# Kernel optimization log

Hardware: AMD Instinct MI355X
Metric: run time of the kernel (lower is better)

## Reference

```python
import jax, jax.numpy as jnp
import numpy as np

T, N, C, S = 512, 32, 5000, 100
BLANK = 0
NEG = -1e30  # log-space 'zero'


def setup_inputs() -> dict:
    key = jax.random.key(0)
    k1, k2, k3 = jax.random.split(key, 3)
    logits = jax.random.normal(k1, (T, N, C), dtype=jnp.float32)
    log_probs = jax.nn.log_softmax(logits, axis=-1)  # CTC expects log-probs
    targets = jax.random.randint(k2, (N, S), 1, C)   # labels never equal blank(=0)
    input_lengths = jnp.full((N,), T, dtype=jnp.int32)
    target_lengths = jax.random.randint(k3, (N,), S // 2, S + 1).astype(jnp.int32)
    return {"log_probs": log_probs, "targets": targets,
            "input_lengths": input_lengths, "target_lengths": target_lengths}


def _logsumexp3(a, b, c):
    m = jnp.maximum(jnp.maximum(a, b), c)
    return m + jnp.log(jnp.exp(a - m) + jnp.exp(b - m) + jnp.exp(c - m))


def _ctc_loss(log_probs, targets, input_lengths, target_lengths, blank=BLANK):
    Tm, Nb, Cc = log_probs.shape
    Sm = targets.shape[1]
    L = 2 * Sm + 1  # extended (blank-interleaved) label lattice width

    # extended targets: [blank, t0, blank, t1, ..., blank]  -> shape [N, L]
    ext = jnp.full((Nb, L), blank, dtype=targets.dtype)
    ext = ext.at[:, 1::2].set(targets)
    is_label = (jnp.arange(L) % 2 == 1)
    ext_prev2 = jnp.concatenate(
        [jnp.full((Nb, 2), -1, dtype=ext.dtype), ext[:, :-2]], axis=1)
    allow_skip = is_label[None, :] & (ext != ext_prev2)          # [N, L]
    pos_mask = jnp.arange(L)[None, :] < (2 * target_lengths + 1)[:, None]

    def emit(lp_t):  # lp_t: [N, C] -> [N, L] gather of label log-probs
        return jnp.take_along_axis(lp_t, ext, axis=1)

    # init alpha at t=0
    e0 = emit(log_probs[0])
    alpha0 = jnp.full((Nb, L), NEG, dtype=log_probs.dtype)
    alpha0 = alpha0.at[:, 0].set(e0[:, 0])
    alpha0 = alpha0.at[:, 1].set(jnp.where(target_lengths > 0, e0[:, 1], NEG))
    alpha0 = jnp.where(pos_mask, alpha0, NEG)

    neg1 = jnp.full((Nb, 1), NEG, dtype=log_probs.dtype)
    neg2 = jnp.full((Nb, 2), NEG, dtype=log_probs.dtype)

    def step(alpha, xs):
        lp_t, t = xs
        a1 = jnp.concatenate([neg1, alpha[:, :-1]], axis=1)
        a2 = jnp.where(allow_skip,
                       jnp.concatenate([neg2, alpha[:, :-2]], axis=1), NEG)
        new = _logsumexp3(alpha, a1, a2) + emit(lp_t)
        new = jnp.where(pos_mask, new, NEG)
        active = (t < input_lengths)[:, None]  # freeze alpha past input length
        return jnp.where(active, new, alpha), None

    alpha, _ = jax.lax.scan(step, alpha0,
                            (log_probs[1:], jnp.arange(1, Tm)))

    # total log-likelihood: last blank + last label states
    last = (2 * target_lengths).astype(jnp.int32)
    a_blank = jnp.take_along_axis(alpha, last[:, None], axis=1)[:, 0]
    a_label = jnp.take_along_axis(alpha, jnp.maximum(last - 1, 0)[:, None], axis=1)[:, 0]
    m = jnp.maximum(a_blank, a_label)
    ll = m + jnp.log(jnp.exp(a_blank - m) + jnp.exp(a_label - m))
    loss = -ll
    # zero_infinity=True: zero out infinite losses
    loss = jnp.where(jnp.isfinite(loss) & (loss < 1e29), loss, 0.0)
    # reduction='mean': divide by target_lengths (clamped to 1), then batch mean
    loss = loss / jnp.maximum(target_lengths, 1).astype(loss.dtype)
    return jnp.mean(loss)


def reference(log_probs, targets, input_lengths, target_lengths):
    return _ctc_loss(log_probs, targets, input_lengths, target_lengths)
```

## Files before the change

kernel.cpp:

```cpp
#include <hip/hip_runtime.h>
#include <cstdint>
#include <cmath>

#define Tt   512
#define Nb   32
#define Cc   5000
#define Sm   100
#define NEGV (-1e30f)
#define LOG2E 1.4426950408889634f
#define LN2   0.6931471805599453f
#define TCH  8

#if __has_builtin(__builtin_amdgcn_exp2f)
#define EXP2F(x) __builtin_amdgcn_exp2f(x)
#else
#define EXP2F(x) exp2f(x)
#endif
#if __has_builtin(__builtin_amdgcn_logf)
#define LOG2F(x) __builtin_amdgcn_logf(x)
#else
#define LOG2F(x) log2f(x)
#endif

__device__ __forceinline__ float lse2_l2(float a, float b) {
    float m = fmaxf(a, b);
    return m + LOG2F(1.0f + EXP2F(fminf(a, b) - m));
}
__device__ __forceinline__ float lse3_l2(float a, float b, float c) {
    float m   = fmaxf(fmaxf(a, b), c);
    float mid = __builtin_amdgcn_fmed3f(a, b, c);
    float lo  = fminf(fminf(a, b), c);
    return m + LOG2F(1.0f + EXP2F(mid - m) + EXP2F(lo - m));
}

__global__ __launch_bounds__(128, 1)
void ctc_gather_kernel(const float* __restrict__ lp,
                       const int*   __restrict__ tgt,
                       float*       __restrict__ em2,
                       float*       __restrict__ out)
{
    const int bid = blockIdx.x;
    const int n   = bid >> 6;
    const int t0  = (bid & 63) * TCH;
    const int j   = threadIdx.x;

    if (bid == 0 && j == 127) out[0] = 0.0f;

    float* dst = em2 + (((size_t)n * Tt + t0) << 7) + j;

    if (j <= Sm) {
        const int e = (j < Sm) ? tgt[n * Sm + j] : 0;
        const float* src = lp + (size_t)n * Cc + e;
        float v[TCH];
#pragma unroll
        for (int k = 0; k < TCH; ++k)
            v[k] = src[(size_t)(t0 + k) * (Nb * Cc)];
#pragma unroll
        for (int k = 0; k < TCH; ++k)
            dst[k << 7] = v[k] * LOG2E;
    } else {
#pragma unroll
        for (int k = 0; k < TCH; ++k)
            dst[k << 7] = NEGV;
    }
}

__global__ __launch_bounds__(64, 1)
void ctc_alpha_wave_kernel(const float* __restrict__ em2,
                           const int*   __restrict__ tgt,
                           const int*   __restrict__ ilen,
                           const int*   __restrict__ tlen,
                           float*       __restrict__ out)
{
    const int n = blockIdx.x;
    const int i = threadIdx.x;

    const int tl = tlen[n];
    const int il = ilen[n];

    const int j1 = 2 * i, j3 = 2 * i + 1;
    bool s1 = false, s3 = false;
    if (j1 >= 1 && j1 < Sm) s1 = (tgt[n * Sm + j1] != tgt[n * Sm + j1 - 1]);
    if (j3 < Sm)            s3 = (tgt[n * Sm + j3] != tgt[n * Sm + j3 - 1]);

    const float2* e2 = (const float2*)em2 + ((size_t)n << 15);

    const int pull = (i > 0 ? i - 1 : 0) << 2;

    float2 E0 = e2[i];
    float b0 = __int_as_float(
        __builtin_amdgcn_readlane(__float_as_int(E0.x), 50));
    float a0 = (i == 0)           ? b0   : NEGV;
    float a1 = (i == 0 && tl > 0) ? E0.x : NEGV;
    float a2 = NEGV;
    float a3 = NEGV;

    constexpr int PF = 8;
    float2 ebuf[PF];
#pragma unroll
    for (int k = 0; k < PF; ++k)
        ebuf[k] = e2[((1 + k) << 6) + i];

    for (int tb = 1; tb < Tt; tb += PF) {
#pragma unroll
        for (int k = 0; k < PF; ++k) {
            const int t = tb + k;
            if (t < Tt) {
                float2 e  = ebuf[k];
                int    tp = t + PF;
                if (tp < Tt) ebuf[k] = e2[(tp << 6) + i];

                float eb = __int_as_float(
                    __builtin_amdgcn_readlane(__float_as_int(e.x), 50));

                float p3  = __int_as_float(
                    __builtin_amdgcn_ds_bpermute(pull, __float_as_int(a3)));
                float am0 = (i > 0) ? p3 : NEGV;

                float n0 = lse2_l2(a0, am0)                   + eb;
                float n1 = lse3_l2(a1, a0, s1 ? p3 : NEGV)    + e.x;
                float n2 = lse2_l2(a2, a1)                    + eb;
                float n3 = lse3_l2(a3, a2, s3 ? a1 : NEGV)    + e.y;

                if (t < il) {
                    a0 = n0; a1 = n1; a2 = n2; a3 = n3;
                }
            }
        }
    }

    const int lb = 2 * tl;
    const int lv = (lb - 1 >= 0) ? lb - 1 : 0;

    int   cb = lb & 3;
    float vb = (cb == 0) ? a0 : (cb == 1) ? a1 : (cb == 2) ? a2 : a3;
    float ab = __shfl(vb, lb >> 2);
    int   cl = lv & 3;
    float vl = (cl == 0) ? a0 : (cl == 1) ? a1 : (cl == 2) ? a2 : a3;
    float al = __shfl(vl, lv >> 2);

    if (i == 0) {
        float m    = fmaxf(ab, al);
        float ll2  = m + LOG2F(EXP2F(ab - m) + EXP2F(al - m));
        float loss = -ll2 * LN2;
        if (!(isfinite(loss) && loss < 1e29f)) loss = 0.0f;
        int   d    = (tl >= 1) ? tl : 1;
        atomicAdd(out, loss / ((float)d * (float)Nb));
    }
}

extern "C" void kernel_launch(void* const* d_in, const int* in_sizes, int n_in,
                              void* d_out, int out_size, void* d_ws, size_t ws_size,
                              hipStream_t stream)
{
    const float* lp   = (const float*)d_in[0];
    const int*   tgt  = (const int*)  d_in[1];
    const int*   ilen = (const int*)  d_in[2];
    const int*   tlen = (const int*)  d_in[3];
    float*       out  = (float*)d_out;

    float* em2 = (float*)d_ws;

    ctc_gather_kernel<<<Nb * (Tt / TCH), 128, 0, stream>>>(lp, tgt, em2, out);
    ctc_alpha_wave_kernel<<<Nb, 64, 0, stream>>>(em2, tgt, ilen, tlen, out);
}
```

Before: 480.1 us.

## Stage full log-prob rows in LDS with coalesced loads before label gather

The gather kernel now assigns one block per (batch, time) row. The block loads the whole 5000-class row with coalesced float4 reads into shared memory, then gathers the label log-probs from LDS. This replaces scattered strided global loads, which are latency-bound, with streaming bandwidth-bound reads. The cost is reading the entire log-prob tensor rather than only the roughly 101 needed entries per row.

```diff
diff --git a/kernel.cpp b/kernel.cpp
--- a/kernel.cpp
+++ b/kernel.cpp
@@ -9,7 +9,6 @@
 #define NEGV (-1e30f)
 #define LOG2E 1.4426950408889634f
 #define LN2   0.6931471805599453f
-#define TCH  8
 
 #if __has_builtin(__builtin_amdgcn_exp2f)
 #define EXP2F(x) __builtin_amdgcn_exp2f(x)
@@ -33,35 +32,40 @@
     return m + LOG2F(1.0f + EXP2F(mid - m) + EXP2F(lo - m));
 }
 
-__global__ __launch_bounds__(128, 1)
+__global__ __launch_bounds__(256, 1)
 void ctc_gather_kernel(const float* __restrict__ lp,
                        const int*   __restrict__ tgt,
                        float*       __restrict__ em2,
                        float*       __restrict__ out)
 {
     const int bid = blockIdx.x;
-    const int n   = bid >> 6;
-    const int t0  = (bid & 63) * TCH;
-    const int j   = threadIdx.x;
+    const int n   = bid >> 9;
+    const int t   = bid & (Tt - 1);
+    const int tid = threadIdx.x;
 
-    if (bid == 0 && j == 127) out[0] = 0.0f;
+    __shared__ float row[Cc];
+    __shared__ int   stgt[Sm];
 
-    float* dst = em2 + (((size_t)n * Tt + t0) << 7) + j;
+    if (bid == 0 && tid == 255) out[0] = 0.0f;
 
-    if (j <= Sm) {
-        const int e = (j < Sm) ? tgt[n * Sm + j] : 0;
-        const float* src = lp + (size_t)n * Cc + e;
-        float v[TCH];
+    const float4* src4 = (const float4*)(lp + ((size_t)t * Nb + n) * Cc);
 #pragma unroll
-        for (int k = 0; k < TCH; ++k)
-            v[k] = src[(size_t)(t0 + k) * (Nb * Cc)];
-#pragma unroll
-        for (int k = 0; k < TCH; ++k)
-            dst[k << 7] = v[k] * LOG2E;
-    } else {
-#pragma unroll
-        for (int k = 0; k < TCH; ++k)
-            dst[k << 7] = NEGV;
+    for (int idx = tid; idx < 1250; idx += 256) {
+        float4 v = src4[idx];
+        row[idx * 4 + 0] = v.x;
+        row[idx * 4 + 1] = v.y;
+        row[idx * 4 + 2] = v.z;
+        row[idx * 4 + 3] = v.w;
+    }
+    if (tid < Sm) stgt[tid] = tgt[n * Sm + tid];
+    __syncthreads();
+
+    if (tid < 128) {
+        float v;
+        if (tid < Sm)       v = row[stgt[tid]] * LOG2E;
+        else if (tid == Sm) v = row[0] * LOG2E;
+        else                v = NEGV;
+        em2[((size_t)bid << 7) + tid] = v;
     }
 }
 
@@ -161,6 +165,6 @@
 
     float* em2 = (float*)d_ws;
 
-    ctc_gather_kernel<<<Nb * (Tt / TCH), 128, 0, stream>>>(lp, tgt, em2, out);
+    ctc_gather_kernel<<<Nb * Tt, 256, 0, stream>>>(lp, tgt, em2, out);
     ctc_alpha_wave_kernel<<<Nb, 64, 0, stream>>>(em2, tgt, ilen, tlen, out);
 }
```

New measurement: 528.2 us. +10.0%, slower.
